# Optimization experiments

Measured on AMD Instinct MI355X. Metric: run time of the kernel, lower is better.

## Reference

```python
import jax, jax.numpy as jnp
import numpy as np

B, C, H, NH = 4, 512, 768, 12        # docs, seq len, hidden, attn heads
NE, MM = 20, 23                      # entities/doc, max mentions/entity
NP_ = NE * (NE - 1)                  # 380 head-tail pairs per doc
QS, POS, EMB, BLK, NB = 128, 128, 768, 64, 12
NCLS = 97
NEG = -10000.0

def _lin(k, i, o):
    return jax.random.normal(k, (i, o), jnp.float32) / np.sqrt(i)

def setup_inputs():
    key = jax.random.key(0)
    ks = jax.random.split(key, 24)
    seq = jax.random.normal(ks[0], (B, C, H), jnp.float32)
    att = jax.random.uniform(ks[1], (B, NH, C, C), jnp.float32)
    midx = jax.random.randint(ks[2], (B, NE, MM), 0, C)
    cnt = jax.random.randint(ks[3], (B, NE), 1, MM + 1)
    mmask = (jnp.arange(MM)[None, None, :] < cnt[:, :, None]).astype(jnp.float32)
    hh, tt = jnp.meshgrid(jnp.arange(NE), jnp.arange(NE), indexing='ij')
    off = ~jnp.eye(NE, dtype=bool)
    hts = jnp.stack([hh[off], tt[off]], -1)
    hts = jnp.broadcast_to(hts[None], (B, NP_, 2))
    vis = (jax.random.uniform(ks[4], (B, NP_, NP_)) > 0.3).astype(jnp.float32)
    inp = dict(sequence_output=seq, attention=att, mention_idx=midx,
               mention_mask=mmask, hts=hts, visible_mask=vis)
    wspec = [('Wcq', H, QS), ('Weq', H, QS), ('Whe', 2 * H, EMB), ('Wte', 2 * H, EMB),
             ('Wbl', EMB * BLK, EMB), ('Wpp', EMB + 2 * POS, EMB),
             ('Wgq', EMB, EMB), ('Wgk', EMB, EMB), ('Wgv', EMB, EMB),
             ('Wp1', 3 * EMB, EMB), ('Wp2', EMB, NCLS)]
    for j, (nm, i, o) in enumerate(wspec):
        inp[nm] = _lin(ks[5 + j], i, o)
        inp['b' + nm[1:]] = jnp.zeros((o,), jnp.float32)
    for nm in ('bgq', 'bgk', 'bgv'):
        inp.pop(nm)
    inp['pos_emb'] = jax.random.normal(ks[20], (42, POS), jnp.float32) * 0.02
    return inp

def reference(sequence_output, attention, mention_idx, mention_mask, hts, visible_mask,
              Wcq, bcq, Weq, beq, Whe, bhe, Wte, bte, Wbl, bbl, Wpp, bpp,
              Wgq, Wgk, Wgv, Wp1, bp1, Wp2, bp2, pos_emb):
    b3 = jnp.arange(B)[:, None, None]
    # per-entity mention gather (padded mentions zeroed, as in the torch loop)
    ent_emb = sequence_output[b3, mention_idx] * mention_mask[..., None]        # [B,NE,MM,H]
    att_t = jnp.transpose(attention, (0, 2, 1, 3))                              # [B,C,NH,C]
    ent_att = att_t[b3, mention_idx] * mention_mask[..., None, None]            # [B,NE,MM,NH,C]
    cnt = mention_mask.sum(-1)[..., None, None]
    ent_att = ent_att.sum(2) / cnt                                              # mean over valid mentions [B,NE,NH,C]

    bi = jnp.arange(B)[:, None]
    hi, ti = hts[..., 0], hts[..., 1]
    hs_m, ts_m = ent_emb[bi, hi], ent_emb[bi, ti]                               # [B,P,MM,H]
    hmask, tmask = mention_mask[bi, hi], mention_mask[bi, ti]                   # [B,P,MM]
    ht_att = (ent_att[bi, hi] * ent_att[bi, ti]).mean(2)                        # mean over heads [B,P,C]
    ht_att = ht_att / (ht_att.sum(-1, keepdims=True) + 1e-5)
    rs = jnp.einsum('bld,bpl->bpd', sequence_output, ht_att)                    # context [B,P,H]

    htq = rs @ Wcq + bcq                                                        # [B,P,QS]
    scale = 1.0 / np.sqrt(EMB)                                                  # original divides by sqrt(emb_size)
    G1 = jnp.einsum('bpq,bpmq->bpm', htq, hs_m @ Weq + beq) * scale
    G2 = jnp.einsum('bpq,bpmq->bpm', htq, ts_m @ Weq + beq) * scale
    G1 = jnp.where(hmask > 0, G1, NEG)
    G2 = jnp.where(tmask > 0, G2, NEG)
    hs = jnp.einsum('bpm,bpmh->bph', jax.nn.softmax(G1, -1), hs_m)
    ts = jnp.einsum('bpm,bpmh->bph', jax.nn.softmax(G2, -1), ts_m)

    hs = jnp.tanh(jnp.concatenate([hs, rs], -1) @ Whe + bhe)                    # [B,P,EMB]
    ts = jnp.tanh(jnp.concatenate([ts, rs], -1) @ Wte + bte)
    bh = hs.reshape(B, NP_, NB, BLK)
    bt = ts.reshape(B, NP_, NB, BLK)
    pair = (bh[..., :, None] * bt[..., None, :]).reshape(B, NP_, EMB * BLK)     # grouped bilinear feature
    pair = pair @ Wbl + bbl                                                     # [B,P,EMB]
    hs_core, ts_core = pos_emb[hi], pos_emb[ti]                                 # [B,P,POS]
    pair = jnp.tanh(jnp.concatenate([hs_core, pair, ts_core], -1) @ Wpp + bpp)

    # pair graph: one masked self-attention layer over pairs with residual
    q, k, v = pair @ Wgq, pair @ Wgk, pair @ Wgv
    sc = jnp.einsum('bpd,bqd->bpq', q, k) / np.sqrt(EMB)
    sc = jnp.where(visible_mask > 0, sc, NEG)
    pair = pair + jnp.einsum('bpq,bqd->bpd', jax.nn.softmax(sc, -1), v)

    feat = jnp.concatenate([hs, ts, pair], -1)                                  # [B,P,3*EMB]
    logits = jnp.tanh(feat @ Wp1 + bp1) @ Wp2 + bp2                             # dropout is identity at eval
    return logits.reshape(B * NP_, NCLS)
```

## Files before the change

### kernel.cpp

```cpp
#include <hip/hip_runtime.h>
#include <hip/hip_bf16.h>

#define Bn   4
#define Cn   512
#define Hn   768
#define NHn  12
#define NEn  20
#define MMn  23
#define Pn   380
#define Mr   1520
#define QSn  128
#define NEGV (-10000.0f)
#define SCL  0.036084391824351615f

typedef unsigned int uint32;
typedef __attribute__((ext_vector_type(4))) float float4v;
typedef __attribute__((ext_vector_type(2))) _Float16 half2v;
typedef __attribute__((ext_vector_type(2))) __fp16 fp16x2;
typedef __attribute__((ext_vector_type(8))) _Float16 half8;

__device__ __forceinline__ unsigned short f2h(float f){
    return __builtin_bit_cast(unsigned short, (_Float16)f);
}
__device__ __forceinline__ uint32 pkrtz(float a, float b){
    fp16x2 h = __builtin_amdgcn_cvt_pkrtz(a, b);
    return __builtin_bit_cast(uint32, h);
}
__device__ __forceinline__ half8 mulsplat(half8 a, uint32 hd){
    half2v s = __builtin_bit_cast(half2v, hd);
    union { half8 h; half2v c[4]; } u, v;
    u.h = a;
    #pragma unroll
    for (int i = 0; i < 4; i++) v.c[i] = u.c[i] * s;
    return v.h;
}

static const size_t o_HS = 0;
static const size_t o_TS = 1167360;
static const size_t o_PB = 2334720;
static const size_t Xo   = 3502080;
static const size_t oEA = Xo;
static const size_t oEE = Xo+491520;
static const size_t oEK = Xo+1904640;
static const size_t oHA = Xo+2140160;
static const size_t oHQ = Xo+2918400;
static const size_t oSH = Xo+3112960;
static const size_t oST = Xo+4280320;
static const size_t oRS = Xo+5447680;
static const size_t oSEQT = Xo+6615040;
static const size_t oWCQ = Xo;
static const size_t oWEQ = Xo+49152;
static const size_t oWHE = Xo;
static const size_t oWTE = Xo+589824;
static const size_t oWBL = Xo;
static const size_t oFP = Xo;
static const size_t oPT = Xo+1556480;
static const size_t oQ  = Xo+2723840;
static const size_t oKT = Xo+3891200;
static const size_t oV  = Xo+5058560;
static const size_t oP2 = Xo+6225920;
static const size_t oT1 = Xo+7393280;
static const size_t oWPP = Xo+8560640;
static const size_t oWGQ = Xo+8953856;
static const size_t oWGK = Xo+9248768;
static const size_t oWGV = Xo+9543680;
static const size_t oWP1 = Xo+9838592;
static const size_t oWP2 = Xo+10723328;


__global__ __launch_bounds__(256) void k_ent_att(const float* __restrict__ att,
    const int* __restrict__ midx, const float* __restrict__ mmask, float* __restrict__ ea)
{
    int x = blockIdx.x;
    int nh = x % NHn; int e = (x / NHn) % NEn; int b = x / (NHn * NEn);
    __shared__ int   sidx[MMn];
    __shared__ float smsk[MMn];
    int t = threadIdx.x;
    if (t < MMn) { sidx[t] = midx[(b*NEn+e)*MMn + t]; smsk[t] = mmask[(b*NEn+e)*MMn + t]; }
    __syncthreads();
    float cnt = 0.f;
    for (int m = 0; m < MMn; m++) cnt += smsk[m];
    for (int c = t; c < Cn; c += 256) {
        float acc = 0.f;
        for (int m = 0; m < MMn; m++)
            acc += smsk[m] * att[((size_t)(b*NHn+nh)*Cn + sidx[m])*Cn + c];
        ea[(size_t)x*Cn + c] = acc / cnt;
    }
}

__global__ __launch_bounds__(256) void k_ent_emb(const float* __restrict__ seq,
    const int* __restrict__ midx, const float* __restrict__ mmask, float* __restrict__ ee)
{
    int x = blockIdx.x;
    int b = x / (NEn*MMn);
    int idx = midx[x]; float msk = mmask[x];
    int t = threadIdx.x;
    for (int h = t; h < Hn; h += 256)
        ee[(size_t)x*Hn + h] = msk * seq[((size_t)b*Cn + idx)*Hn + h];
}

__global__ __launch_bounds__(256) void k_htatt(const float* __restrict__ ea,
    const int* __restrict__ hts, float* __restrict__ hta)
{
    int row = blockIdx.x; int b = row / Pn;
    int he = hts[row*2], te = hts[row*2+1];
    __shared__ float sc[Cn];
    __shared__ float red[256];
    int t = threadIdx.x;
    const float* eah = ea + (size_t)(b*NEn+he)*NHn*Cn;
    const float* eat = ea + (size_t)(b*NEn+te)*NHn*Cn;
    for (int c = t; c < Cn; c += 256) {
        float a = 0.f;
        for (int nh = 0; nh < NHn; nh++) a += eah[nh*Cn+c]*eat[nh*Cn+c];
        sc[c] = a * (1.0f/NHn);
    }
    __syncthreads();
    float ps = sc[t] + sc[t+256];
    red[t] = ps; __syncthreads();
    for (int s = 128; s > 0; s >>= 1) { if (t < s) red[t] += red[t+s]; __syncthreads(); }
    float inv = 1.0f/(red[0] + 1e-5f);
    for (int c = t; c < Cn; c += 256) hta[(size_t)row*Cn + c] = sc[c]*inv;
}

__global__ __launch_bounds__(256) void k_select(const float* __restrict__ htq,
    const float* __restrict__ ekey, const float* __restrict__ ee,
    const float* __restrict__ mmask, const int* __restrict__ hts,
    float* __restrict__ selh, float* __restrict__ selt)
{
    int row = blockIdx.x; int side = blockIdx.y;
    int b = row / Pn;
    int e = hts[row*2 + side];
    __shared__ float qv[QSn];
    __shared__ float gsc[MMn];
    __shared__ float ew[MMn];
    int t = threadIdx.x;
    if (t < QSn) qv[t] = htq[(size_t)row*QSn + t];
    __syncthreads();
    if (t < MMn) {
        const float* kr = ekey + ((size_t)(b*NEn+e)*MMn + t)*QSn;
        float g = 0.f;
        for (int qq = 0; qq < QSn; qq++) g += qv[qq]*kr[qq];
        g *= SCL;
        float msk = mmask[(b*NEn+e)*MMn + t];
        gsc[t] = (msk > 0.f) ? g : NEGV;
    }
    __syncthreads();
    float mx = -1e30f;
    for (int m = 0; m < MMn; m++) mx = fmaxf(mx, gsc[m]);
    if (t < MMn) ew[t] = expf(gsc[t] - mx);
    __syncthreads();
    float s = 0.f;
    for (int m = 0; m < MMn; m++) s += ew[m];
    float invs = 1.0f/s;
    float* dst = side ? selt : selh;
    const float* eb = ee + (size_t)(b*NEn+e)*MMn*Hn;
    for (int h = t; h < Hn; h += 256) {
        float o = 0.f;
        for (int m = 0; m < MMn; m++) o += ew[m]*eb[(size_t)m*Hn + h];
        dst[(size_t)row*Hn + h] = o*invs;
    }
}

struct WD { const float* src; unsigned short* dst; int K; int N; int Npad; int t0; };
struct WT8 { WD d[8]; int nd; };

__global__ __launch_bounds__(256) void k_wtr(WT8 tab)
{
    int b = blockIdx.x;
    int i = 0;
    while (i+1 < tab.nd && b >= tab.d[i+1].t0) i++;
    WD d = tab.d[i];
    int tile = b - d.t0;
    int ktiles = d.K >> 6;
    int kt = tile % ktiles, nt = tile / ktiles;
    int k0 = kt*64, n0 = nt*64;
    __shared__ __align__(16) unsigned short tl[64][72];
    int t = threadIdx.x;
    int nl = t & 63, rq = t >> 6;
    #pragma unroll
    for (int r = 0; r < 16; r++) {
        int kl = r*4 + rq;
        float v = (n0+nl < d.N) ? d.src[(size_t)(k0+kl)*d.N + n0 + nl] : 0.f;
        tl[nl][kl] = f2h(v);
    }
    __syncthreads();
    int nn2 = t >> 2, kk0 = (t & 3) * 16;
    uint4 a = *(const uint4*)&tl[nn2][kk0];
    uint4 bq = *(const uint4*)&tl[nn2][kk0+8];
    uint4* dst = (uint4*)&d.dst[(size_t)(n0+nn2)*d.K + k0 + kk0];
    dst[0] = a; dst[1] = bq;
}

template<int MODE, int TM>
__global__ __launch_bounds__(256,4) void k_gmfma(
    const float* __restrict__ A0, const float* __restrict__ A1, const float* __restrict__ A2,
    int KA, int KB, int KC,
    const unsigned short* __restrict__ Wt,
    const float* __restrict__ bias, float* __restrict__ out,
    float* __restrict__ out2, float* __restrict__ out3,
    int Mtot, int N, int kchunk,
    long aStride, long wStride, long oStride)
{
    __shared__ __align__(16) unsigned short sa[64][72];
    __shared__ __align__(16) unsigned short sw[64][72];
    int t = threadIdx.x;
    int K = KA + KB + KC;
    int row0 = blockIdx.x * 64;
    int n0 = blockIdx.y * 64;
    int bz = blockIdx.z;
    const float* Ab = A0; const unsigned short* W = Wt; float* O = out;
    if (MODE & 32) { Ab += (size_t)bz*aStride; W += (size_t)bz*wStride; O += (size_t)bz*oStride; }
    int k0 = 0, k1 = K;
    if (MODE & 1) { k0 = bz*kchunk; k1 = k0 + kchunk; }
    int lane = t & 63, w = t >> 6, ln = lane & 15, q = lane >> 4;
    int sr = t >> 2;
    int sk = (t & 3) * 16;
    int rA = row0 + sr; if (rA > Mtot-1) rA = Mtot-1;

    float4v acc[4];
    #pragma unroll
    for (int mt = 0; mt < 4; mt++) acc[mt] = (float4v)0.f;

    for (int kk = k0; kk < k1; kk += 64) {
        const float* src; int kloc, Kl, seg;
        if (kk < KA)            { src = Ab; kloc = kk;          Kl = KA; seg = 0; }
        else if (kk < KA + KB)  { src = A1; kloc = kk - KA;     Kl = KB; seg = 1; }
        else                    { src = A2; kloc = kk - KA - KB; Kl = KC; seg = 2; }
        const float* ap = &src[(size_t)rA*Kl + kloc + sk];
        float4 v0 = ((const float4*)ap)[0];
        float4 v1 = ((const float4*)ap)[1];
        float4 v2 = ((const float4*)ap)[2];
        float4 v3 = ((const float4*)ap)[3];
        if (TM && ((TM >> seg) & 1)) {
            v0.x = tanhf(v0.x); v0.y = tanhf(v0.y); v0.z = tanhf(v0.z); v0.w = tanhf(v0.w);
            v1.x = tanhf(v1.x); v1.y = tanhf(v1.y); v1.z = tanhf(v1.z); v1.w = tanhf(v1.w);
            v2.x = tanhf(v2.x); v2.y = tanhf(v2.y); v2.z = tanhf(v2.z); v2.w = tanhf(v2.w);
            v3.x = tanhf(v3.x); v3.y = tanhf(v3.y); v3.z = tanhf(v3.z); v3.w = tanhf(v3.w);
        }
        const uint4* gw = (const uint4*)&W[(size_t)(n0+sr)*K + kk + sk];
        uint4 w0 = gw[0], w1 = gw[1];
        uint4 pa, pb;
        pa.x = pkrtz(v0.x, v0.y); pa.y = pkrtz(v0.z, v0.w);
        pa.z = pkrtz(v1.x, v1.y); pa.w = pkrtz(v1.z, v1.w);
        pb.x = pkrtz(v2.x, v2.y); pb.y = pkrtz(v2.z, v2.w);
        pb.z = pkrtz(v3.x, v3.y); pb.w = pkrtz(v3.z, v3.w);
        *(uint4*)&sa[sr][sk]   = pa;
        *(uint4*)&sa[sr][sk+8] = pb;
        *(uint4*)&sw[sr][sk]   = w0;
        *(uint4*)&sw[sr][sk+8] = w1;
        __syncthreads();
        half8 b0 = *(const half8*)&sw[w*16+ln][q*8];
        half8 b1 = *(const half8*)&sw[w*16+ln][32 + q*8];
        #pragma unroll
        for (int mt = 0; mt < 4; mt++) {
            half8 a0 = *(const half8*)&sa[mt*16+ln][q*8];
            half8 a1 = *(const half8*)&sa[mt*16+ln][32 + q*8];
            acc[mt] = __builtin_amdgcn_mfma_f32_16x16x32_f16(a0, b0, acc[mt], 0, 0, 0);
            acc[mt] = __builtin_amdgcn_mfma_f32_16x16x32_f16(a1, b1, acc[mt], 0, 0, 0);
        }
        __syncthreads();
    }
    int nn = n0 + w*16 + ln;
    if (MODE & 16) {
        int sg = nn / Hn; int nl = nn - sg*Hn;
        #pragma unroll
        for (int mt = 0; mt < 4; mt++) {
            #pragma unroll
            for (int r = 0; r < 4; r++) {
                int row = row0 + mt*16 + q*4 + r;
                if (row >= Mtot) continue;
                float val = acc[mt][r];
                if (sg == 0)      out [(size_t)row*Hn + nl] = val;
                else if (sg == 2) out3[(size_t)row*Hn + nl] = val;
                else {
                    int bb = row / Pn, pp = row % Pn;
                    out2[((size_t)bb*Hn + nl)*Pn + pp] = val;
                }
            }
        }
        return;
    }
    if (nn >= N) return;
    float bv = (MODE & 4) ? bias[nn] : 0.f;
    #pragma unroll
    for (int mt = 0; mt < 4; mt++) {
        #pragma unroll
        for (int r = 0; r < 4; r++) {
            int row = row0 + mt*16 + q*4 + r;
            if (row >= Mtot) continue;
            float val = acc[mt][r];
            if (MODE & 1) atomicAdd(&O[(size_t)row*N + nn], val);
            else          O[(size_t)row*N + nn] = val + bv;
        }
    }
}

__global__ __launch_bounds__(256) void k_binit(const float* __restrict__ bias,
    float* __restrict__ o, int N)
{
    int idx = blockIdx.x*256 + threadIdx.x;
    o[idx] = bias[idx % N];
}

__global__ __launch_bounds__(256) void k_binit3(const float* __restrict__ b0,
    const float* __restrict__ b1, const float* __restrict__ b2, float* __restrict__ o)
{
    int idx = blockIdx.x*256 + threadIdx.x;
    int r = idx / (Mr*Hn);
    const float* bb = (r == 0) ? b0 : ((r == 1) ? b1 : b2);
    o[idx] = bb[idx % Hn];
}

__global__ __launch_bounds__(256,3) void k_blmfma(const float* __restrict__ hs,
    const float* __restrict__ ts, const unsigned short* __restrict__ Wt,
    float* __restrict__ pb)
{
    __shared__ __align__(16) unsigned short hsl[2][64][72];
    __shared__ __align__(16) unsigned short tsl[2][64][72];
    int t = threadIdx.x;
    int bid = blockIdx.x + 24*(blockIdx.y + 6*(int)blockIdx.z);
    int sb = (bid & 7)*108 + (bid >> 3);
    int p_t = sb % 24; int r2 = sb / 24;
    int p0 = p_t * 64;
    int d0 = (r2 % 6) * 128;
    int g  = r2 / 6;
    int lane = t & 63, w = t >> 6, ln = lane & 15, q = lane >> 4;

    {
        int p = t & 63; int s = t >> 6;
        int nn = s >> 1; int c0 = (s & 1) * 32;
        int pr = p0 + p; if (pr > Mr-1) pr = Mr-1;
        int n = 2*g + nn;
        const float* hp = hs + (size_t)pr*Hn + n*64 + c0;
        const float* tp = ts + (size_t)pr*Hn + n*64 + c0;
        #pragma unroll
        for (int b2 = 0; b2 < 2; b2++) {
            const float4* hp4 = (const float4*)(hp + b2*16);
            const float4* tp4 = (const float4*)(tp + b2*16);
            float4 x0=hp4[0], x1=hp4[1], x2=hp4[2], x3=hp4[3];
            uint4 oh, oh2;
            oh.x = pkrtz(tanhf(x0.x),tanhf(x0.y)); oh.y = pkrtz(tanhf(x0.z),tanhf(x0.w));
            oh.z = pkrtz(tanhf(x1.x),tanhf(x1.y)); oh.w = pkrtz(tanhf(x1.z),tanhf(x1.w));
            oh2.x = pkrtz(tanhf(x2.x),tanhf(x2.y)); oh2.y = pkrtz(tanhf(x2.z),tanhf(x2.w));
            oh2.z = pkrtz(tanhf(x3.x),tanhf(x3.y)); oh2.w = pkrtz(tanhf(x3.z),tanhf(x3.w));
            *(uint4*)&hsl[nn][p][c0 + b2*16]     = oh;
            *(uint4*)&hsl[nn][p][c0 + b2*16 + 8] = oh2;
            float4 y0=tp4[0], y1=tp4[1], y2=tp4[2], y3=tp4[3];
            uint4 ot, ot2;
            ot.x = pkrtz(tanhf(y0.x),tanhf(y0.y)); ot.y = pkrtz(tanhf(y0.z),tanhf(y0.w));
            ot.z = pkrtz(tanhf(y1.x),tanhf(y1.y)); ot.w = pkrtz(tanhf(y1.z),tanhf(y1.w));
            ot2.x = pkrtz(tanhf(y2.x),tanhf(y2.y)); ot2.y = pkrtz(tanhf(y2.z),tanhf(y2.w));
            ot2.z = pkrtz(tanhf(y3.x),tanhf(y3.y)); ot2.w = pkrtz(tanhf(y3.z),tanhf(y3.w));
            *(uint4*)&tsl[nn][p][c0 + b2*16]     = ot;
            *(uint4*)&tsl[nn][p][c0 + b2*16 + 8] = ot2;
        }
    }
    __syncthreads();

    float4v acc[4][2];
    #pragma unroll
    for (int e = 0; e < 4; e++)
        #pragma unroll
        for (int f = 0; f < 2; f++) acc[e][f] = (float4v)0.f;

    const unsigned short* wrow0 = Wt + (size_t)(d0 + w*32 + ln)*49152 + q*8;
    const unsigned short* wrow1 = wrow0 + (size_t)16*49152;

    #pragma unroll
    for (int nn = 0; nn < 2; nn++) {
        int n = 2*g + nn;
        const unsigned short* wp0 = wrow0 + (size_t)n*4096;
        const unsigned short* wp1 = wrow1 + (size_t)n*4096;
        const unsigned short* hrow = &hsl[nn][ln][0];
        half8 tsr[4][2];
        #pragma unroll
        for (int e = 0; e < 4; e++) {
            tsr[e][0] = *(const half8*)&tsl[nn][e*16+ln][q*8];
            tsr[e][1] = *(const half8*)&tsl[nn][e*16+ln][32 + q*8];
        }
        uint4 a0A[4], a1A[4]; uint32 hwA[4];
        uint4 a0B[4], a1B[4]; uint32 hwB[4];
        #pragma unroll
        for (int c = 0; c < 4; c++) {
            a0A[c] = *(const uint4*)(wp0 + c*32);
            a1A[c] = *(const uint4*)(wp1 + c*32);
        }
        #pragma unroll
        for (int e = 0; e < 4; e++) hwA[e] = *(const uint32*)(hrow + e*1152);

        for (int i0 = 0; i0 < 64; i0 += 4) {
            #pragma unroll
            for (int c = 0; c < 4; c++) {
                a0B[c] = *(const uint4*)(wp0 + (i0+2)*64 + c*32);
                a1B[c] = *(const uint4*)(wp1 + (i0+2)*64 + c*32);
            }
            #pragma unroll
            for (int e = 0; e < 4; e++) hwB[e] = *(const uint32*)(hrow + e*1152 + (i0+2));
            #pragma unroll
            for (int c = 0; c < 4; c++) {
                #pragma unroll
                for (int e = 0; e < 4; e++) {
                    uint32 hd = __builtin_amdgcn_perm(hwA[e], hwA[e],
                                                      (c & 2) ? 0x03020302u : 0x01000100u);
                    half8 bfr = mulsplat(tsr[e][c & 1], hd);
                    acc[e][0] = __builtin_amdgcn_mfma_f32_16x16x32_f16(
                        __builtin_bit_cast(half8, a0A[c]), bfr, acc[e][0], 0, 0, 0);
                    acc[e][1] = __builtin_amdgcn_mfma_f32_16x16x32_f16(
                        __builtin_bit_cast(half8, a1A[c]), bfr, acc[e][1], 0, 0, 0);
                }
            }
            if (i0 + 4 < 64) {
                #pragma unroll
                for (int c = 0; c < 4; c++) {
                    a0A[c] = *(const uint4*)(wp0 + (i0+4)*64 + c*32);
                    a1A[c] = *(const uint4*)(wp1 + (i0+4)*64 + c*32);
                }
                #pragma unroll
                for (int e = 0; e < 4; e++) hwA[e] = *(const uint32*)(hrow + e*1152 + (i0+4));
            }
            #pragma unroll
            for (int c = 0; c < 4; c++) {
                #pragma unroll
                for (int e = 0; e < 4; e++) {
                    uint32 hd = __builtin_amdgcn_perm(hwB[e], hwB[e],
                                                      (c & 2) ? 0x03020302u : 0x01000100u);
                    half8 bfr = mulsplat(tsr[e][c & 1], hd);
                    acc[e][0] = __builtin_amdgcn_mfma_f32_16x16x32_f16(
                        __builtin_bit_cast(half8, a0B[c]), bfr, acc[e][0], 0, 0, 0);
                    acc[e][1] = __builtin_amdgcn_mfma_f32_16x16x32_f16(
                        __builtin_bit_cast(half8, a1B[c]), bfr, acc[e][1], 0, 0, 0);
                }
            }
        }
    }
    #pragma unroll
    for (int e = 0; e < 4; e++) {
        int p = p0 + e*16 + ln;
        if (p >= Mr) continue;
        #pragma unroll
        for (int f = 0; f < 2; f++) {
            int dbase = d0 + w*32 + f*16 + q*4;
            #pragma unroll
            for (int r = 0; r < 4; r++)
                atomicAdd(&pb[(size_t)p*Hn + dbase + r], acc[e][f][r]);
        }
    }
}


__global__ __launch_bounds__(256) void k_featpp(const float* __restrict__ pairbl,
    const float* __restrict__ pos, const int* __restrict__ hts, float* __restrict__ fpp)
{
    int row = blockIdx.x; int t = threadIdx.x;
    int he = hts[row*2], te = hts[row*2+1];
    float* dst = fpp + (size_t)row*1024;
    if (t < 128) { dst[t] = pos[he*128 + t]; dst[896 + t] = pos[te*128 + t]; }
    for (int h = t; h < Hn; h += 256) dst[128 + h] = pairbl[(size_t)row*Hn + h];
}

__global__ __launch_bounds__(256) void k_graph(const float* __restrict__ q,
    const float* __restrict__ kT, const float* __restrict__ v, const float* __restrict__ vis,
    const float* __restrict__ pairT, float* __restrict__ pair2)
{
    int row = blockIdx.x; int b = row / Pn; int p = row % Pn;
    __shared__ float qs[Hn];
    __shared__ float sc[Pn];
    __shared__ float red[256];
    int t = threadIdx.x;
    for (int h = t; h < Hn; h += 256) qs[h] = q[(size_t)row*Hn + h];
    __syncthreads();
    for (int qq = t; qq < Pn; qq += 256) {
        const float* kcol = kT + (size_t)b*Hn*Pn + qq;
        float a = 0.f;
        for (int h = 0; h < Hn; h++) a += qs[h]*kcol[(size_t)h*Pn];
        a *= SCL;
        float ms = vis[((size_t)b*Pn + p)*Pn + qq];
        sc[qq] = (ms > 0.f) ? a : NEGV;
    }
    __syncthreads();
    float mx = -1e30f;
    for (int qq = t; qq < Pn; qq += 256) mx = fmaxf(mx, sc[qq]);
    red[t] = mx; __syncthreads();
    for (int s = 128; s > 0; s >>= 1) { if (t < s) red[t] = fmaxf(red[t], red[t+s]); __syncthreads(); }
    mx = red[0];
    __syncthreads();
    float ps = 0.f;
    for (int qq = t; qq < Pn; qq += 256) { float e2 = expf(sc[qq]-mx); sc[qq] = e2; ps += e2; }
    red[t] = ps; __syncthreads();
    for (int s = 128; s > 0; s >>= 1) { if (t < s) red[t] += red[t+s]; __syncthreads(); }
    float invs = 1.0f/red[0];
    __syncthreads();
    float a0 = 0.f, a1 = 0.f, a2 = 0.f;
    for (int qq = 0; qq < Pn; qq++) {
        float sv = sc[qq];
        const float* vr = v + ((size_t)b*Pn+qq)*Hn + t;
        a0 += sv*vr[0]; a1 += sv*vr[256]; a2 += sv*vr[512];
    }
    const float* pt = pairT + (size_t)row*Hn + t;
    float* o = pair2 + (size_t)row*Hn + t;
    o[0]   = tanhf(pt[0])   + a0*invs;
    o[256] = tanhf(pt[256]) + a1*invs;
    o[512] = tanhf(pt[512]) + a2*invs;
}

__global__ __launch_bounds__(256) void k_fillu(unsigned int* p, unsigned int v, int n){
    int i = blockIdx.x*256 + threadIdx.x;
    if (i < n) p[i] = v;
}

extern "C" void kernel_launch(void* const* d_in, const int* in_sizes, int n_in,
                              void* d_out, int out_size, void* d_ws, size_t ws_size,
                              hipStream_t stream)
{
    const float* seq  = (const float*)d_in[0];
    const float* att  = (const float*)d_in[1];
    const int*   midx = (const int*)d_in[2];
    const float* mmask= (const float*)d_in[3];
    const int*   hts  = (const int*)d_in[4];
    const float* vis  = (const float*)d_in[5];
    const float* Wcq = (const float*)d_in[6];  const float* bcq = (const float*)d_in[7];
    const float* Weq = (const float*)d_in[8];  const float* beq = (const float*)d_in[9];
    const float* Whe = (const float*)d_in[10]; const float* bhe = (const float*)d_in[11];
    const float* Wte = (const float*)d_in[12]; const float* bte = (const float*)d_in[13];
    const float* Wbl = (const float*)d_in[14]; const float* bbl = (const float*)d_in[15];
    const float* Wpp = (const float*)d_in[16]; const float* bpp = (const float*)d_in[17];
    const float* Wgq = (const float*)d_in[18];
    const float* Wgk = (const float*)d_in[19];
    const float* Wgv = (const float*)d_in[20];
    const float* Wp1 = (const float*)d_in[21]; const float* bp1 = (const float*)d_in[22];
    const float* Wp2 = (const float*)d_in[23]; const float* bp2 = (const float*)d_in[24];
    const float* pos = (const float*)d_in[25];
    float* ws = (float*)d_ws;
    float* out = (float*)d_out;
    const float* nul = nullptr;
    float* nulw = nullptr;

    if (ws_size < 89505792ULL) {
        int n = out_size/2;
        k_fillu<<<(n+255)/256, 256, 0, stream>>>((unsigned int*)d_out, 0x476A476Au, n);
        return;
    }

    unsigned short* WCQt = (unsigned short*)(ws + oWCQ);
    unsigned short* WEQt = (unsigned short*)(ws + oWEQ);
    unsigned short* SEQt = (unsigned short*)(ws + oSEQT);
    unsigned short* WHEt = (unsigned short*)(ws + oWHE);
    unsigned short* WTEt = (unsigned short*)(ws + oWTE);
    unsigned short* WBLt = (unsigned short*)(ws + oWBL);
    unsigned short* WPPt = (unsigned short*)(ws + oWPP);
    unsigned short* WGQt = (unsigned short*)(ws + oWGQ);
    unsigned short* WP1t = (unsigned short*)(ws + oWP1);
    unsigned short* WP2t = (unsigned short*)(ws + oWP2);

    k_ent_att<<<Bn*NEn*NHn, 256, 0, stream>>>(att, midx, mmask, ws + oEA);
    k_ent_emb<<<Bn*NEn*MMn, 256, 0, stream>>>(seq, midx, mmask, ws + oEE);
    k_htatt<<<Mr, 256, 0, stream>>>(ws + oEA, hts, ws + oHA);

    {
        WT8 tb{}; tb.nd = 6;
        tb.d[0] = { Wcq, WCQt, 768, 128, 128, 0 };
        tb.d[1] = { Weq, WEQt, 768, 128, 128, 24 };
        for (int b = 0; b < 4; b++)
            tb.d[2+b] = { seq + (size_t)b*Cn*Hn, SEQt + (size_t)b*Hn*Cn, Cn, Hn, Hn, 48 + b*96 };
        k_wtr<<<432, 256, 0, stream>>>(tb);
    }
    k_gmfma<32,0><<<dim3(6,12,4), 256, 0, stream>>>(ws + oHA, nul, nul, Cn, 0, 0,
        SEQt, nul, ws + oRS, nulw, nulw, Pn, Hn, 0,
        (long)Pn*Cn, (long)Hn*Cn, (long)Pn*Hn);
    k_gmfma<4,0><<<dim3(24,2,1), 256, 0, stream>>>(ws + oRS, nul, nul, Hn, 0, 0,
        WCQt, bcq, ws + oHQ, nulw, nulw, Mr, QSn, 0, 0, 0, 0);
    k_gmfma<4,0><<<dim3(29,2,1), 256, 0, stream>>>(ws + oEE, nul, nul, Hn, 0, 0,
        WEQt, beq, ws + oEK, nulw, nulw, Bn*NEn*MMn, QSn, 0, 0, 0, 0);
    k_select<<<dim3(Mr,2), 256, 0, stream>>>(ws + oHQ, ws + oEK, ws + oEE,
        mmask, hts, ws + oSH, ws + oST);

    {
        WT8 tb{}; tb.nd = 2;
        tb.d[0] = { Whe, WHEt, 1536, 768, 768, 0 };
        tb.d[1] = { Wte, WTEt, 1536, 768, 768, 288 };
        k_wtr<<<576, 256, 0, stream>>>(tb);
    }
    k_binit3<<<(3*Mr*Hn)/256, 256, 0, stream>>>(bhe, bte, bbl, ws + o_HS);
    k_gmfma<1,0><<<dim3(24,12,3), 256, 0, stream>>>(ws + oSH, ws + oRS, nul, Hn, Hn, 0,
        WHEt, nul, ws + o_HS, nulw, nulw, Mr, Hn, 512, 0, 0, 0);
    k_gmfma<1,0><<<dim3(24,12,3), 256, 0, stream>>>(ws + oST, ws + oRS, nul, Hn, Hn, 0,
        WTEt, nul, ws + o_TS, nulw, nulw, Mr, Hn, 512, 0, 0, 0);

    {
        WT8 tb{}; tb.nd = 1;
        tb.d[0] = { Wbl, WBLt, 49152, 768, 768, 0 };
        k_wtr<<<9216, 256, 0, stream>>>(tb);
    }
    k_blmfma<<<dim3(24,6,6), 256, 0, stream>>>(ws + o_HS, ws + o_TS, WBLt, ws + o_PB);

    k_featpp<<<Mr, 256, 0, stream>>>(ws + o_PB, pos, hts, ws + oFP);

    {
        WT8 tb{}; tb.nd = 6;
        tb.d[0] = { Wpp, WPPt, 1024, 768, 768, 0 };
        tb.d[1] = { Wgq, WGQt, 768, 768, 768, 192 };
        tb.d[2] = { Wgk, (unsigned short*)(ws + oWGK), 768, 768, 768, 336 };
        tb.d[3] = { Wgv, (unsigned short*)(ws + oWGV), 768, 768, 768, 480 };
        tb.d[4] = { Wp1, WP1t, 2304, 768, 768, 624 };
        tb.d[5] = { Wp2, WP2t, 768, 97, 128, 1056 };
        k_wtr<<<1080, 256, 0, stream>>>(tb);
    }
    k_binit<<<(Mr*Hn)/256, 256, 0, stream>>>(bpp, ws + oPT, Hn);
    k_gmfma<1,0><<<dim3(24,12,2), 256, 0, stream>>>(ws + oFP, nul, nul, 1024, 0, 0,
        WPPt, nul, ws + oPT, nulw, nulw, Mr, Hn, 512, 0, 0, 0);
    k_gmfma<16,1><<<dim3(24,36,1), 256, 0, stream>>>(ws + oPT, nul, nul, Hn, 0, 0,
        WGQt, nul, ws + oQ, ws + oKT, ws + oV, Mr, 3*Hn, 0, 0, 0, 0);
    k_graph<<<Mr, 256, 0, stream>>>(ws + oQ, ws + oKT, ws + oV, vis, ws + oPT, ws + oP2);
    k_binit<<<(Mr*Hn)/256, 256, 0, stream>>>(bp1, ws + oT1, Hn);
    k_gmfma<1,3><<<dim3(24,12,3), 256, 0, stream>>>(ws + o_HS, ws + o_TS, ws + oP2,
        Hn, Hn, Hn, WP1t, nul, ws + oT1, nulw, nulw, Mr, Hn, 768, 0, 0, 0);
    k_gmfma<4,1><<<dim3(24,2,1), 256, 0, stream>>>(ws + oT1, nul, nul, Hn, 0, 0,
        WP2t, bp2, out, nulw, nulw, Mr, 97, 0, 0, 0, 0);
}
```

Measured before the change: 1.039 ms.

## Stage bilinear weight tiles into LDS with async global_load_lds double buffering

The grouped-bilinear MFMA kernel now streams weight tiles through a double-buffered LDS buffer using direct global-to-LDS loads, instead of each wave loading weights from global memory into registers. It XOR-swizzles the LDS layouts to avoid bank conflicts and halves the output tile width per block, doubling the grid. The goal is to cut redundant per-lane global weight traffic and register pressure. In exchange it adds a barrier every k-step and doubles the atomicAdd-contending blocks and the re-computed tanh staging of hs and ts.

Measured after the change: 1.024 ms. No clear change (-1.5%).

```diff
diff --git a/kernel.cpp b/kernel.cpp
--- a/kernel.cpp
+++ b/kernel.cpp
@@ -33,6 +33,11 @@
     #pragma unroll
     for (int i = 0; i < 4; i++) v.c[i] = u.c[i] * s;
     return v.h;
+}
+__device__ __forceinline__ void gl_lds16(const unsigned short* g, unsigned short* l){
+    __builtin_amdgcn_global_load_lds(
+        (const __attribute__((address_space(1))) void*)g,
+        (__attribute__((address_space(3))) void*)l, 16, 0, 0);
 }
 
 static const size_t o_HS = 0;
@@ -315,20 +320,37 @@
     const float* __restrict__ ts, const unsigned short* __restrict__ Wt,
     float* __restrict__ pb)
 {
-    __shared__ __align__(16) unsigned short hsl[2][64][72];
-    __shared__ __align__(16) unsigned short tsl[2][64][72];
-    int t = threadIdx.x;
-    int bid = blockIdx.x + 24*(blockIdx.y + 6*(int)blockIdx.z);
-    int sb = (bid & 7)*108 + (bid >> 3);
+    __shared__ __align__(16) unsigned short hsl[2][64][64];
+    __shared__ __align__(16) unsigned short tsl[2][64][64];
+    __shared__ __align__(16) unsigned short wbuf[2][64][64];
+    int t = threadIdx.x;
+    int bid = blockIdx.x + 24*(blockIdx.y + 12*(int)blockIdx.z);
+    int sb = (bid & 7)*216 + (bid >> 3);
     int p_t = sb % 24; int r2 = sb / 24;
     int p0 = p_t * 64;
-    int d0 = (r2 % 6) * 128;
-    int g  = r2 / 6;
+    int d0 = (r2 % 12) * 64;
+    int g  = r2 / 12;
     int lane = t & 63, w = t >> 6, ln = lane & 15, q = lane >> 4;
+    int xr = (ln & 7) << 3;
+
+    const unsigned short* Wd = Wt + (size_t)d0*49152;
+    auto stage = [&](int cc, int bufi){
+        int n2 = 2*g + (cc >> 6);
+        size_t kb = (size_t)n2*4096 + (size_t)(cc & 63)*64;
+        #pragma unroll
+        for (int pass = 0; pass < 2; pass++) {
+            int r = pass*32 + (t >> 3);
+            int c0s = (t & 7) * 8;
+            gl_lds16(Wd + (size_t)r*49152 + kb + (c0s ^ ((r & 7) << 3)),
+                     &wbuf[bufi][r][c0s]);
+        }
+    };
+    stage(0, 0);
 
     {
         int p = t & 63; int s = t >> 6;
         int nn = s >> 1; int c0 = (s & 1) * 32;
+        int xw = (p & 7) << 3;
         int pr = p0 + p; if (pr > Mr-1) pr = Mr-1;
         int n = 2*g + nn;
         const float* hp = hs + (size_t)pr*Hn + n*64 + c0;
@@ -343,107 +365,63 @@
             oh.z = pkrtz(tanhf(x1.x),tanhf(x1.y)); oh.w = pkrtz(tanhf(x1.z),tanhf(x1.w));
             oh2.x = pkrtz(tanhf(x2.x),tanhf(x2.y)); oh2.y = pkrtz(tanhf(x2.z),tanhf(x2.w));
             oh2.z = pkrtz(tanhf(x3.x),tanhf(x3.y)); oh2.w = pkrtz(tanhf(x3.z),tanhf(x3.w));
-            *(uint4*)&hsl[nn][p][c0 + b2*16]     = oh;
-            *(uint4*)&hsl[nn][p][c0 + b2*16 + 8] = oh2;
+            *(uint4*)&hsl[nn][p][(c0 + b2*16)     ^ xw] = oh;
+            *(uint4*)&hsl[nn][p][(c0 + b2*16 + 8) ^ xw] = oh2;
             float4 y0=tp4[0], y1=tp4[1], y2=tp4[2], y3=tp4[3];
             uint4 ot, ot2;
             ot.x = pkrtz(tanhf(y0.x),tanhf(y0.y)); ot.y = pkrtz(tanhf(y0.z),tanhf(y0.w));
             ot.z = pkrtz(tanhf(y1.x),tanhf(y1.y)); ot.w = pkrtz(tanhf(y1.z),tanhf(y1.w));
             ot2.x = pkrtz(tanhf(y2.x),tanhf(y2.y)); ot2.y = pkrtz(tanhf(y2.z),tanhf(y2.w));
             ot2.z = pkrtz(tanhf(y3.x),tanhf(y3.y)); ot2.w = pkrtz(tanhf(y3.z),tanhf(y3.w));
-            *(uint4*)&tsl[nn][p][c0 + b2*16]     = ot;
-            *(uint4*)&tsl[nn][p][c0 + b2*16 + 8] = ot2;
-        }
-    }
-    __syncthreads();
-
-    float4v acc[4][2];
-    #pragma unroll
-    for (int e = 0; e < 4; e++)
-        #pragma unroll
-        for (int f = 0; f < 2; f++) acc[e][f] = (float4v)0.f;
-
-    const unsigned short* wrow0 = Wt + (size_t)(d0 + w*32 + ln)*49152 + q*8;
-    const unsigned short* wrow1 = wrow0 + (size_t)16*49152;
-
+            *(uint4*)&tsl[nn][p][(c0 + b2*16)     ^ xw] = ot;
+            *(uint4*)&tsl[nn][p][(c0 + b2*16 + 8) ^ xw] = ot2;
+        }
+    }
+    __syncthreads();
+
+    float4v acc[4];
+    #pragma unroll
+    for (int e = 0; e < 4; e++) acc[e] = (float4v)0.f;
+
+    int buf = 0;
     #pragma unroll
     for (int nn = 0; nn < 2; nn++) {
-        int n = 2*g + nn;
-        const unsigned short* wp0 = wrow0 + (size_t)n*4096;
-        const unsigned short* wp1 = wrow1 + (size_t)n*4096;
-        const unsigned short* hrow = &hsl[nn][ln][0];
-        half8 tsr[4][2];
+        half8 tsr0[4], tsr1[4];
         #pragma unroll
         for (int e = 0; e < 4; e++) {
-            tsr[e][0] = *(const half8*)&tsl[nn][e*16+ln][q*8];
-            tsr[e][1] = *(const half8*)&tsl[nn][e*16+ln][32 + q*8];
-        }
-        uint4 a0A[4], a1A[4]; uint32 hwA[4];
-        uint4 a0B[4], a1B[4]; uint32 hwB[4];
-        #pragma unroll
-        for (int c = 0; c < 4; c++) {
-            a0A[c] = *(const uint4*)(wp0 + c*32);
-            a1A[c] = *(const uint4*)(wp1 + c*32);
-        }
-        #pragma unroll
-        for (int e = 0; e < 4; e++) hwA[e] = *(const uint32*)(hrow + e*1152);
-
-        for (int i0 = 0; i0 < 64; i0 += 4) {
+            tsr0[e] = *(const half8*)&tsl[nn][e*16+ln][(q*8) ^ xr];
+            tsr1[e] = *(const half8*)&tsl[nn][e*16+ln][(32 + q*8) ^ xr];
+        }
+        for (int ci = 0; ci < 64; ci++) {
+            int cc = nn*64 + ci;
+            if (cc + 1 < 128) stage(cc+1, buf^1);
+            uint32 hd[4];
             #pragma unroll
-            for (int c = 0; c < 4; c++) {
-                a0B[c] = *(const uint4*)(wp0 + (i0+2)*64 + c*32);
-                a1B[c] = *(const uint4*)(wp1 + (i0+2)*64 + c*32);
+            for (int e = 0; e < 4; e++) {
+                uint32 hv = hsl[nn][e*16+ln][ci ^ xr];
+                hd[e] = __builtin_amdgcn_perm(hv, hv, 0x01000100u);
             }
             #pragma unroll
-            for (int e = 0; e < 4; e++) hwB[e] = *(const uint32*)(hrow + e*1152 + (i0+2));
-            #pragma unroll
-            for (int c = 0; c < 4; c++) {
+            for (int c = 0; c < 2; c++) {
+                half8 wf = *(const half8*)&wbuf[buf][w*16+ln][(c*32 + q*8) ^ xr];
                 #pragma unroll
                 for (int e = 0; e < 4; e++) {
-                    uint32 hd = __builtin_amdgcn_perm(hwA[e], hwA[e],
-                                                      (c & 2) ? 0x03020302u : 0x01000100u);
-                    half8 bfr = mulsplat(tsr[e][c & 1], hd);
-                    acc[e][0] = __builtin_amdgcn_mfma_f32_16x16x32_f16(
-                        __builtin_bit_cast(half8, a0A[c]), bfr, acc[e][0], 0, 0, 0);
-                    acc[e][1] = __builtin_amdgcn_mfma_f32_16x16x32_f16(
-                        __builtin_bit_cast(half8, a1A[c]), bfr, acc[e][1], 0, 0, 0);
+                    half8 bfr = mulsplat(c ? tsr1[e] : tsr0[e], hd[e]);
+                    acc[e] = __builtin_amdgcn_mfma_f32_16x16x32_f16(wf, bfr, acc[e], 0, 0, 0);
                 }
             }
-            if (i0 + 4 < 64) {
-                #pragma unroll
-                for (int c = 0; c < 4; c++) {
-                    a0A[c] = *(const uint4*)(wp0 + (i0+4)*64 + c*32);
-                    a1A[c] = *(const uint4*)(wp1 + (i0+4)*64 + c*32);
-                }
-                #pragma unroll
-                for (int e = 0; e < 4; e++) hwA[e] = *(const uint32*)(hrow + e*1152 + (i0+4));
-            }
-            #pragma unroll
-            for (int c = 0; c < 4; c++) {
-                #pragma unroll
-                for (int e = 0; e < 4; e++) {
-                    uint32 hd = __builtin_amdgcn_perm(hwB[e], hwB[e],
-                                                      (c & 2) ? 0x03020302u : 0x01000100u);
-                    half8 bfr = mulsplat(tsr[e][c & 1], hd);
-                    acc[e][0] = __builtin_amdgcn_mfma_f32_16x16x32_f16(
-                        __builtin_bit_cast(half8, a0B[c]), bfr, acc[e][0], 0, 0, 0);
-                    acc[e][1] = __builtin_amdgcn_mfma_f32_16x16x32_f16(
-                        __builtin_bit_cast(half8, a1B[c]), bfr, acc[e][1], 0, 0, 0);
-                }
-            }
+            __syncthreads();
+            buf ^= 1;
         }
     }
     #pragma unroll
     for (int e = 0; e < 4; e++) {
         int p = p0 + e*16 + ln;
         if (p >= Mr) continue;
-        #pragma unroll
-        for (int f = 0; f < 2; f++) {
-            int dbase = d0 + w*32 + f*16 + q*4;
-            #pragma unroll
-            for (int r = 0; r < 4; r++)
-                atomicAdd(&pb[(size_t)p*Hn + dbase + r], acc[e][f][r]);
-        }
+        int dbase = d0 + w*16 + q*4;
+        #pragma unroll
+        for (int r = 0; r < 4; r++)
+            atomicAdd(&pb[(size_t)p*Hn + dbase + r], acc[e][r]);
     }
 }
 
@@ -591,7 +569,7 @@
         tb.d[0] = { Wbl, WBLt, 49152, 768, 768, 0 };
         k_wtr<<<9216, 256, 0, stream>>>(tb);
     }
-    k_blmfma<<<dim3(24,6,6), 256, 0, stream>>>(ws + o_HS, ws + o_TS, WBLt, ws + o_PB);
+    k_blmfma<<<dim3(24,12,6), 256, 0, stream>>>(ws + o_HS, ws + o_TS, WBLt, ws + o_PB);
 
     k_featpp<<<Mr, 256, 0, stream>>>(ws + o_PB, pos, hts, ws + oFP);
 
```
